# Optimization experiments

Measured on AMD Instinct MI355X. Metric: run time of the kernel, lower is better.

The kernel has to match this reference:

```python
import jax, jax.numpy as jnp
import numpy as np

NUM_EMBEDDINGS = 1024  # K
EMBEDDING_DIM = 64     # D
COMMITMENT_COST = 0.25


def setup_inputs() -> dict:
    key = jax.random.key(0)
    k1, k2 = jax.random.split(key)
    inputs = jax.random.normal(k1, (16, 4096, EMBEDDING_DIM), dtype=jnp.float32)
    # codebook init: uniform(-1/K, 1/K) as in nn.Embedding init in the module
    embedding = jax.random.uniform(
        k2, (NUM_EMBEDDINGS, EMBEDDING_DIM), dtype=jnp.float32,
        minval=-1.0 / NUM_EMBEDDINGS, maxval=1.0 / NUM_EMBEDDINGS)
    return {"inputs": inputs, "embedding": embedding}


def reference(inputs, embedding):
    input_shape = inputs.shape
    K = embedding.shape[0]
    flat = inputs.reshape(-1, embedding.shape[1])  # [N, D]

    distances = (jnp.sum(flat * flat, axis=1, keepdims=True)
                 + jnp.sum(embedding * embedding, axis=1)
                 - 2.0 * jnp.einsum('nd,kd->nk', flat, embedding))
    idx = jnp.argmin(distances, axis=1)                      # [N]
    encodings = jax.nn.one_hot(idx, K, dtype=flat.dtype)     # [N, K]
    quantized = embedding[idx]                               # [N, D] gather

    codebook_loss = jnp.mean((jax.lax.stop_gradient(quantized) - flat) ** 2)
    commitment_loss = jnp.mean((quantized - jax.lax.stop_gradient(flat)) ** 2)
    loss = codebook_loss + COMMITMENT_COST * commitment_loss

    # straight-through estimator
    quantized_st = flat + jax.lax.stop_gradient(quantized - flat)

    quantized_st = quantized_st.reshape(input_shape)
    encodings = encodings.reshape(*input_shape[:-1], K)
    return (quantized_st, encodings, loss, codebook_loss, commitment_loss)
```

## Files before the change

### kernel.cpp

```cpp
#include <hip/hip_runtime.h>
#include <float.h>

#define NVEC 65536
#define KCB  1024
#define DIM  64
#define ENC_OFF   ((size_t)NVEC * DIM)
#define LOSS_OFF  (ENC_OFF + (size_t)NVEC * KCB)
#define BAND 6e-5f

#define WS_SE_BOFF  64
#define WS_EH_BOFF  8192
#define WS_EL_BOFF  (8192 + 131072)
#define WS_IDX_BOFF (WS_EL_BOFF + 131072)

typedef __attribute__((ext_vector_type(8))) short short8;
typedef __attribute__((ext_vector_type(4))) float f32x4;

__device__ __forceinline__ unsigned short f2bf(float f) {
    unsigned u = __float_as_uint(f);
    return (unsigned short)((u + 0x7FFFu + ((u >> 16) & 1u)) >> 16);
}
__device__ __forceinline__ float bf2f(unsigned short h) {
    return __uint_as_float((unsigned)h << 16);
}

__global__ __launch_bounds__(256) void vq_prep(const float* __restrict__ emb,
                                               float* __restrict__ se,
                                               unsigned short* __restrict__ eh,
                                               unsigned short* __restrict__ el,
                                               float* __restrict__ loss3) {
    int g = blockIdx.x * 256 + threadIdx.x;
    if (g < 3) loss3[g] = 0.0f;
    if (g < KCB) {
        const f32x4* er = (const f32x4*)(emb + (size_t)g * DIM);
        double s0 = 0.0, s1 = 0.0, s2 = 0.0, s3 = 0.0;
#pragma unroll
        for (int i = 0; i < 16; i++) {
            f32x4 e = er[i];
            s0 = fma((double)e.x, (double)e.x, s0);
            s1 = fma((double)e.y, (double)e.y, s1);
            s2 = fma((double)e.z, (double)e.z, s2);
            s3 = fma((double)e.w, (double)e.w, s3);
        }
        se[g] = (float)((s0 + s1) + (s2 + s3));
    }
    for (int i = g; i < KCB * DIM; i += 64 * 256) {
        float v = emb[i];
        unsigned short h = f2bf(v);
        eh[i] = h;
        el[i] = f2bf(v - bf2f(h));
    }
}

__global__ __launch_bounds__(256) void vq_screen(const float* __restrict__ x,
                                                 const float* __restrict__ emb,
                                                 const float* __restrict__ se,
                                                 const unsigned short* __restrict__ eh,
                                                 const unsigned short* __restrict__ el,
                                                 unsigned short* __restrict__ idxg) {
    __shared__ float sse[KCB];
    __shared__ int   sidx[128];
    __shared__ int   sflag[128];
    __shared__ int   scnt;
    __shared__ float sxrow[4][64];

    const int tid = threadIdx.x;
    const int wave = tid >> 6, lane = tid & 63;
    const int q = lane >> 4, c = lane & 15;

    if (tid == 0) scnt = 0;
    for (int t = tid; t < KCB; t += 256) sse[t] = se[t];

    const int rowbase = blockIdx.x * 128 + wave * 32;
    short8 ah0[2], ah1[2], al0[2], al1[2];
#pragma unroll
    for (int s = 0; s < 2; s++) {
        float xa[16];
        const f32x4* xp = (const f32x4*)(x + (size_t)(rowbase + s * 16 + c) * DIM);
        ((f32x4*)xa)[0] = xp[2 * q];
        ((f32x4*)xa)[1] = xp[2 * q + 1];
        ((f32x4*)xa)[2] = xp[8 + 2 * q];
        ((f32x4*)xa)[3] = xp[8 + 2 * q + 1];
#pragma unroll
        for (int j = 0; j < 8; j++) {
            unsigned short h0 = f2bf(xa[j]);
            ah0[s][j] = (short)h0;
            al0[s][j] = (short)f2bf(xa[j] - bf2f(h0));
            unsigned short h1 = f2bf(xa[8 + j]);
            ah1[s][j] = (short)h1;
            al1[s][j] = (short)f2bf(xa[8 + j] - bf2f(h1));
        }
    }
    __syncthreads();

    float b1[2][4], b2[2][4];
    int i1[2][4];
#pragma unroll
    for (int s = 0; s < 2; s++)
#pragma unroll
        for (int r = 0; r < 4; r++) { b1[s][r] = FLT_MAX; b2[s][r] = FLT_MAX; i1[s][r] = 0; }

    const unsigned short* ehq = eh + q * 8;
    const unsigned short* elq = el + q * 8;
#pragma unroll 2
    for (int t = 0; t < 64; t++) {
        int kcur = t * 16 + c;
        const unsigned short* bph = ehq + ((size_t)kcur << 6);
        const unsigned short* bpl = elq + ((size_t)kcur << 6);
        short8 bh0 = *(const short8*)bph;
        short8 bh1 = *(const short8*)(bph + 32);
        short8 bl0 = *(const short8*)bpl;
        short8 bl1 = *(const short8*)(bpl + 32);
        float sek = sse[kcur];
#pragma unroll
        for (int s = 0; s < 2; s++) {
            f32x4 acc = {0.f, 0.f, 0.f, 0.f};
            acc = __builtin_amdgcn_mfma_f32_16x16x32_bf16(ah0[s], bh0, acc, 0, 0, 0);
            acc = __builtin_amdgcn_mfma_f32_16x16x32_bf16(ah1[s], bh1, acc, 0, 0, 0);
            acc = __builtin_amdgcn_mfma_f32_16x16x32_bf16(ah0[s], bl0, acc, 0, 0, 0);
            acc = __builtin_amdgcn_mfma_f32_16x16x32_bf16(ah1[s], bl1, acc, 0, 0, 0);
            acc = __builtin_amdgcn_mfma_f32_16x16x32_bf16(al0[s], bh0, acc, 0, 0, 0);
            acc = __builtin_amdgcn_mfma_f32_16x16x32_bf16(al1[s], bh1, acc, 0, 0, 0);
#pragma unroll
            for (int r = 0; r < 4; r++) {
                float v = fmaf(-2.f, acc[r], sek);
                bool lt = v < b1[s][r];
                b2[s][r] = fminf(fmaxf(v, b1[s][r]), b2[s][r]);
                b1[s][r] = lt ? v : b1[s][r];
                i1[s][r] = lt ? kcur : i1[s][r];
            }
        }
    }

#pragma unroll
    for (int m = 1; m <= 8; m <<= 1) {
#pragma unroll
        for (int s = 0; s < 2; s++)
#pragma unroll
            for (int r = 0; r < 4; r++) {
                float ob1 = __shfl_xor(b1[s][r], m, 64);
                float ob2 = __shfl_xor(b2[s][r], m, 64);
                int oi = __shfl_xor(i1[s][r], m, 64);
                float nb2 = fminf(fmaxf(b1[s][r], ob1), fminf(b2[s][r], ob2));
                if (ob1 < b1[s][r]) { b1[s][r] = ob1; i1[s][r] = oi; }
                b2[s][r] = nb2;
            }
    }
    if (c == 0) {
#pragma unroll
        for (int s = 0; s < 2; s++)
#pragma unroll
            for (int r = 0; r < 4; r++) {
                int row = wave * 32 + s * 16 + q * 4 + r;
                sidx[row] = i1[s][r];
                if (b2[s][r] - b1[s][r] < BAND) {
                    int p = atomicAdd(&scnt, 1);
                    sflag[p] = row;
                }
            }
    }
    __syncthreads();

    int cnt = scnt;
    for (int f = wave; f < cnt; f += 4) {
        int row = sflag[f];
        int n = blockIdx.x * 128 + row;
        if (lane < 16)
            ((f32x4*)sxrow[wave])[lane] = ((const f32x4*)(x + (size_t)n * DIM))[lane];
        const float* xr = sxrow[wave];

        float r8[8];
#pragma unroll
        for (int j = 0; j < 8; j++) r8[j] = 0.0f;
#pragma unroll
        for (int b = 0; b < 8; b++)
#pragma unroll
            for (int j = 0; j < 8; j++)
                r8[j] = __fadd_rn(r8[j], __fmul_rn(xr[8 * b + j], xr[8 * b + j]));
        float sx = __fadd_rn(
            __fadd_rn(__fadd_rn(r8[0], r8[1]), __fadd_rn(r8[2], r8[3])),
            __fadd_rn(__fadd_rn(r8[4], r8[5]), __fadd_rn(r8[6], r8[7])));

        float bd = FLT_MAX;
        int bk = lane * 16;
        for (int cc = 0; cc < 16; cc++) {
            int k = lane * 16 + cc;
            const f32x4* er = (const f32x4*)(emb + (size_t)k * DIM);
            double s0 = 0.0, s1 = 0.0, s2 = 0.0, s3 = 0.0;
#pragma unroll
            for (int i = 0; i < 16; i++) {
                f32x4 e = er[i];
                f32x4 xv = ((const f32x4*)xr)[i];
                s0 = fma((double)e.x, (double)xv.x, s0);
                s1 = fma((double)e.y, (double)xv.y, s1);
                s2 = fma((double)e.z, (double)xv.z, s2);
                s3 = fma((double)e.w, (double)xv.w, s3);
            }
            float dot32 = (float)((s0 + s1) + (s2 + s3));
            float t1 = __fadd_rn(sx, sse[k]);
            float d = __fsub_rn(t1, __fmul_rn(2.0f, dot32));
            if (d < bd) { bd = d; bk = k; }
        }
        for (int off = 32; off; off >>= 1) {
            float od = __shfl_down(bd, off);
            int ok = __shfl_down(bk, off);
            if (od < bd || (od == bd && ok < bk)) { bd = od; bk = ok; }
        }
        if (lane == 0) sidx[row] = bk;
    }
    __syncthreads();

    if (tid < 128)
        idxg[blockIdx.x * 128 + tid] = (unsigned short)sidx[tid];
}

__global__ __launch_bounds__(256) void vq_write(const float* __restrict__ x,
                                                const float* __restrict__ emb,
                                                const unsigned short* __restrict__ idxg,
                                                float* __restrict__ outq,
                                                float* __restrict__ enc,
                                                float* __restrict__ lossacc) {
    __shared__ int sidx[64];
    __shared__ float red[4];
    const int tid = threadIdx.x;
    if (tid < 64) sidx[tid] = idxg[blockIdx.x * 64 + tid];
    __syncthreads();

    {
        int vec = tid >> 2, ch = tid & 3;
        int id = sidx[vec];
        const f32x4* ebp = (const f32x4*)(emb + (size_t)id * DIM) + ch * 4;
        const f32x4* xp = (const f32x4*)(x + (size_t)(blockIdx.x * 64 + vec) * DIM) + ch * 4;
        f32x4* op = (f32x4*)(outq + (size_t)(blockIdx.x * 64 + vec) * DIM) + ch * 4;
        float sq = 0.0f;
#pragma unroll
        for (int i = 0; i < 4; i++) {
            f32x4 e = ebp[i];
            f32x4 xv = xp[i];
            f32x4 d = e - xv;
            sq += d.x * d.x + d.y * d.y + d.z * d.z + d.w * d.w;
            __builtin_nontemporal_store(e, op + i);
        }
        for (int off = 32; off; off >>= 1) sq += __shfl_down(sq, off);
        if ((tid & 63) == 0) red[tid >> 6] = sq;
        __syncthreads();
        if (tid == 0) atomicAdd(lossacc, red[0] + red[1] + red[2] + red[3]);
    }

    f32x4* encb = (f32x4*)enc + (size_t)blockIdx.x * 64 * 256;
    for (int t = tid; t < 64 * 256; t += 256) {
        int id = sidx[t >> 8];
        int j = (t & 255) << 2;
        f32x4 v;
        v.x = (id == j + 0) ? 1.0f : 0.0f;
        v.y = (id == j + 1) ? 1.0f : 0.0f;
        v.z = (id == j + 2) ? 1.0f : 0.0f;
        v.w = (id == j + 3) ? 1.0f : 0.0f;
        __builtin_nontemporal_store(v, encb + t);
    }
}

__global__ void vq_fin(float* __restrict__ loss3) {
    if (threadIdx.x == 0 && blockIdx.x == 0) {
        float m = loss3[1] * (1.0f / (float)((size_t)NVEC * DIM));
        loss3[0] = 1.25f * m;
        loss3[1] = m;
        loss3[2] = m;
    }
}

extern "C" void kernel_launch(void* const* d_in, const int* in_sizes, int n_in,
                              void* d_out, int out_size, void* d_ws, size_t ws_size,
                              hipStream_t stream) {
    const float* x = (const float*)d_in[0];
    const float* emb = (const float*)d_in[1];
    float* out = (float*)d_out;
    float* se = (float*)((char*)d_ws + WS_SE_BOFF);
    unsigned short* eh = (unsigned short*)((char*)d_ws + WS_EH_BOFF);
    unsigned short* el = (unsigned short*)((char*)d_ws + WS_EL_BOFF);
    unsigned short* idxg = (unsigned short*)((char*)d_ws + WS_IDX_BOFF);

    hipLaunchKernelGGL(vq_prep, dim3(64), dim3(256), 0, stream,
                       emb, se, eh, el, out + LOSS_OFF);
    hipLaunchKernelGGL(vq_screen, dim3(NVEC / 128), dim3(256), 0, stream,
                       x, emb, se, eh, el, idxg);
    hipLaunchKernelGGL(vq_write, dim3(NVEC / 64), dim3(256), 0, stream,
                       x, emb, idxg, out, out + ENC_OFF, out + LOSS_OFF + 1);
    hipLaunchKernelGGL(vq_fin, dim3(1), dim3(64), 0, stream, out + LOSS_OFF);
}
```

Before: 485.0 us.

## Pre-swizzle bf16 hi/lo codebook into MFMA fragment order and use single-wave blocks

The prep kernel now writes the split bf16 codebook in the exact per-lane fragment order the MFMA loop consumes, so each lane's four operand loads per step are contiguous and coalesced instead of strided across codebook rows. The screen kernel changes from 256-thread blocks of 128 rows to 64-thread single-wave blocks of 32 rows, with the loop unrolled by 4. The aim is better memory access and more independent blocks to schedule. The cost is that each block reloads the 1024-entry norm table into shared memory, which is four times as many loads in total. The fp64 refinement of ambiguous rows is now serialized with barriers inside one wave.

```diff
diff --git a/kernel.cpp b/kernel.cpp
--- a/kernel.cpp
+++ b/kernel.cpp
@@ -8,10 +8,9 @@
 #define LOSS_OFF  (ENC_OFF + (size_t)NVEC * KCB)
 #define BAND 6e-5f
 
-#define WS_SE_BOFF  64
-#define WS_EH_BOFF  8192
-#define WS_EL_BOFF  (8192 + 131072)
-#define WS_IDX_BOFF (WS_EL_BOFF + 131072)
+#define WS_SE_BOFF   64
+#define WS_FB_BOFF   8192
+#define WS_IDX_BOFF  (8192 + 262144)
 
 typedef __attribute__((ext_vector_type(8))) short short8;
 typedef __attribute__((ext_vector_type(4))) float f32x4;
@@ -26,8 +25,7 @@
 
 __global__ __launch_bounds__(256) void vq_prep(const float* __restrict__ emb,
                                                float* __restrict__ se,
-                                               unsigned short* __restrict__ eh,
-                                               unsigned short* __restrict__ el,
+                                               unsigned short* __restrict__ fbuf,
                                                float* __restrict__ loss3) {
     int g = blockIdx.x * 256 + threadIdx.x;
     if (g < 3) loss3[g] = 0.0f;
@@ -44,34 +42,41 @@
         }
         se[g] = (float)((s0 + s1) + (s2 + s3));
     }
-    for (int i = g; i < KCB * DIM; i += 64 * 256) {
-        float v = emb[i];
-        unsigned short h = f2bf(v);
-        eh[i] = h;
-        el[i] = f2bf(v - bf2f(h));
-    }
-}
-
-__global__ __launch_bounds__(256) void vq_screen(const float* __restrict__ x,
-                                                 const float* __restrict__ emb,
-                                                 const float* __restrict__ se,
-                                                 const unsigned short* __restrict__ eh,
-                                                 const unsigned short* __restrict__ el,
-                                                 unsigned short* __restrict__ idxg) {
+    {
+        int t = g >> 8, i = (g >> 6) & 3, l = g & 63;
+        int c = l & 15, q = l >> 4;
+        int k = t * 16 + c;
+        int d0 = (i & 1) * 32 + q * 8;
+        const float* src = emb + (size_t)k * DIM + d0;
+        short8 v;
+#pragma unroll
+        for (int j = 0; j < 8; j++) {
+            float f = src[j];
+            unsigned short h = f2bf(f);
+            v[j] = (i < 2) ? (short)h : (short)f2bf(f - bf2f(h));
+        }
+        *(short8*)(fbuf + (size_t)g * 8) = v;
+    }
+}
+
+__global__ __launch_bounds__(64, 4) void vq_screen(const float* __restrict__ x,
+                                                   const float* __restrict__ emb,
+                                                   const float* __restrict__ se,
+                                                   const unsigned short* __restrict__ fbuf,
+                                                   unsigned short* __restrict__ idxg) {
     __shared__ float sse[KCB];
-    __shared__ int   sidx[128];
-    __shared__ int   sflag[128];
+    __shared__ int   sidx[32];
+    __shared__ int   sflag[32];
     __shared__ int   scnt;
-    __shared__ float sxrow[4][64];
-
-    const int tid = threadIdx.x;
-    const int wave = tid >> 6, lane = tid & 63;
+    __shared__ float sxrow[64];
+
+    const int lane = threadIdx.x;
     const int q = lane >> 4, c = lane & 15;
 
-    if (tid == 0) scnt = 0;
-    for (int t = tid; t < KCB; t += 256) sse[t] = se[t];
-
-    const int rowbase = blockIdx.x * 128 + wave * 32;
+    if (lane == 0) scnt = 0;
+    for (int t = lane; t < KCB; t += 64) sse[t] = se[t];
+
+    const int rowbase = blockIdx.x * 32;
     short8 ah0[2], ah1[2], al0[2], al1[2];
 #pragma unroll
     for (int s = 0; s < 2; s++) {
@@ -100,17 +105,15 @@
 #pragma unroll
         for (int r = 0; r < 4; r++) { b1[s][r] = FLT_MAX; b2[s][r] = FLT_MAX; i1[s][r] = 0; }
 
-    const unsigned short* ehq = eh + q * 8;
-    const unsigned short* elq = el + q * 8;
-#pragma unroll 2
+    const unsigned short* fb = fbuf + (size_t)lane * 8;
+#pragma unroll 4
     for (int t = 0; t < 64; t++) {
+        const unsigned short* fbt = fb + t * 2048;
+        short8 bh0 = *(const short8*)(fbt);
+        short8 bh1 = *(const short8*)(fbt + 512);
+        short8 bl0 = *(const short8*)(fbt + 1024);
+        short8 bl1 = *(const short8*)(fbt + 1536);
         int kcur = t * 16 + c;
-        const unsigned short* bph = ehq + ((size_t)kcur << 6);
-        const unsigned short* bpl = elq + ((size_t)kcur << 6);
-        short8 bh0 = *(const short8*)bph;
-        short8 bh1 = *(const short8*)(bph + 32);
-        short8 bl0 = *(const short8*)bpl;
-        short8 bl1 = *(const short8*)(bpl + 32);
         float sek = sse[kcur];
 #pragma unroll
         for (int s = 0; s < 2; s++) {
@@ -151,7 +154,7 @@
         for (int s = 0; s < 2; s++)
 #pragma unroll
             for (int r = 0; r < 4; r++) {
-                int row = wave * 32 + s * 16 + q * 4 + r;
+                int row = s * 16 + q * 4 + r;
                 sidx[row] = i1[s][r];
                 if (b2[s][r] - b1[s][r] < BAND) {
                     int p = atomicAdd(&scnt, 1);
@@ -162,12 +165,13 @@
     __syncthreads();
 
     int cnt = scnt;
-    for (int f = wave; f < cnt; f += 4) {
+    for (int f = 0; f < cnt; f++) {
         int row = sflag[f];
-        int n = blockIdx.x * 128 + row;
+        int n = rowbase + row;
         if (lane < 16)
-            ((f32x4*)sxrow[wave])[lane] = ((const f32x4*)(x + (size_t)n * DIM))[lane];
-        const float* xr = sxrow[wave];
+            ((f32x4*)sxrow)[lane] = ((const f32x4*)(x + (size_t)n * DIM))[lane];
+        __syncthreads();
+        const float* xr = sxrow;
 
         float r8[8];
 #pragma unroll
@@ -207,11 +211,11 @@
             if (od < bd || (od == bd && ok < bk)) { bd = od; bk = ok; }
         }
         if (lane == 0) sidx[row] = bk;
-    }
-    __syncthreads();
-
-    if (tid < 128)
-        idxg[blockIdx.x * 128 + tid] = (unsigned short)sidx[tid];
+        __syncthreads();
+    }
+
+    if (lane < 32)
+        idxg[rowbase + lane] = (unsigned short)sidx[lane];
 }
 
 __global__ __launch_bounds__(256) void vq_write(const float* __restrict__ x,
@@ -276,14 +280,13 @@
     const float* emb = (const float*)d_in[1];
     float* out = (float*)d_out;
     float* se = (float*)((char*)d_ws + WS_SE_BOFF);
-    unsigned short* eh = (unsigned short*)((char*)d_ws + WS_EH_BOFF);
-    unsigned short* el = (unsigned short*)((char*)d_ws + WS_EL_BOFF);
+    unsigned short* fbuf = (unsigned short*)((char*)d_ws + WS_FB_BOFF);
     unsigned short* idxg = (unsigned short*)((char*)d_ws + WS_IDX_BOFF);
 
     hipLaunchKernelGGL(vq_prep, dim3(64), dim3(256), 0, stream,
-                       emb, se, eh, el, out + LOSS_OFF);
-    hipLaunchKernelGGL(vq_screen, dim3(NVEC / 128), dim3(256), 0, stream,
-                       x, emb, se, eh, el, idxg);
+                       emb, se, fbuf, out + LOSS_OFF);
+    hipLaunchKernelGGL(vq_screen, dim3(NVEC / 32), dim3(64), 0, stream,
+                       x, emb, se, fbuf, idxg);
     hipLaunchKernelGGL(vq_write, dim3(NVEC / 64), dim3(256), 0, stream,
                        x, emb, idxg, out, out + ENC_OFF, out + LOSS_OFF + 1);
     hipLaunchKernelGGL(vq_fin, dim3(1), dim3(64), 0, stream, out + LOSS_OFF);
```

New measurement: 604.1 us. 24.6% more time.
